# Performance work log

Measured on AMD Instinct MI355X. Metric: run time of the kernel, lower is better.

Reference implementation:

```python
import jax, jax.numpy as jnp
import numpy as np


def setup_inputs() -> dict:
    key = jax.random.key(0)
    k1, k2, k3, k4, k5 = jax.random.split(key, 5)
    B, C, H, W = 2, 3, 64, 64
    f_tar = jax.random.normal(k1, (B, C, H, W), dtype=jnp.float32)
    f_src = jax.random.normal(k2, (B, C, H, W), dtype=jnp.float32)
    # Pinhole intrinsics (focal=50, principal point at image center) + small noise,
    # guaranteed invertible.
    K_base = jnp.array([[50.0, 0.0, 32.0], [0.0, 50.0, 32.0], [0.0, 0.0, 1.0]],
                       dtype=jnp.float32)
    K = K_base[None] + 0.05 * jax.random.normal(k3, (B, 3, 3), dtype=jnp.float32)
    # Near-identity rotation-like matrix.
    R = jnp.eye(3, dtype=jnp.float32)[None] + 0.1 * jax.random.normal(
        k4, (B, 3, 3), dtype=jnp.float32)
    t = jax.random.normal(k5, (B, 3, 1), dtype=jnp.float32)
    return {"f_tar": f_tar, "f_src": f_src, "K": K, "R": R, "t": t}


def reference(f_tar, f_src, K, R, t):
    B, C, H, W = f_src.shape  # C == 3 (required by the cross product)
    N = H * W
    dtype = f_src.dtype

    f_src_flat = f_src.reshape(B, C, N)  # (B, 3, N)
    f_tar_flat = f_tar.reshape(B, C, N)  # (B, 3, N)

    # A[b, i, j] = <f_src[:, i], f_tar[:, j]>  -> (B, N, N)
    A = jnp.einsum('bci,bcj->bij', f_src_flat, f_tar_flat)

    # Homogeneous pixel coordinates (3, N): rows of meshgrid(H, W, indexing='ij').
    ix, iy = jnp.meshgrid(jnp.arange(H), jnp.arange(W), indexing='ij')
    pix = jnp.stack([ix.reshape(-1), iy.reshape(-1), jnp.ones(N, dtype=jnp.int32)],
                    axis=0).astype(dtype)  # (3, N)

    K_inv = jnp.linalg.inv(K)  # (B, 3, 3)
    # tar_proj = K @ (R @ (K^-1 @ x) + t)   -> (B, 3, N)
    cam_rays = jnp.einsum('bij,jn->bin', K_inv, pix)
    tar_proj = jnp.einsum('bij,bjn->bin', K, jnp.einsum('bij,bjn->bin', R, cam_rays) + t)
    # Origin projects to K @ (R @ 0 + t) = K @ t, broadcast over N.
    o_proj = jnp.einsum('bij,bjn->bin', K, t)  # (B, 3, 1)

    diff = tar_proj - o_proj  # (B, 3, N)

    # Epipolar distance: || (f_src - o) x diff || / ||diff||, broadcast to (B, N, N).
    a = f_src_flat[:, :, :, None] - o_proj[:, :, :, None]  # (B, 3, N, 1)
    b = diff[:, :, None, :]                                 # (B, 3, 1, N)
    cross = jnp.cross(a, b, axis=1)                         # (B, 3, N, N)
    cross_norm = jnp.linalg.norm(cross, axis=1)             # (B, N, N)
    diff_norm = jnp.linalg.norm(diff, axis=1, keepdims=True)  # (B, 1, N)
    d_epipolar = cross_norm / diff_norm                     # (B, N, N)

    # 'sigmoid' in the original is nn.Softmax(dim=-1).
    EPI_THRESH = 0.5
    SHARPNESS = 50.0
    weight_map = 1.0 - jax.nn.softmax(SHARPNESS * (d_epipolar - EPI_THRESH), axis=-1)

    A_weighted = A * weight_map
    attention_map = jax.nn.softmax(A_weighted, axis=1)  # normalize over src positions

    # (B, N, N) @ (B, N, C) -> (B, N, C), then raw view back to (B, C, H, W)
    attended = jnp.einsum('bik,bck->bic', attention_map, f_src_flat)
    return attended.reshape(B, C, H, W)
```

## Files before the change

kernel.cpp:

```cpp
#include <hip/hip_runtime.h>
#include <hip/hip_bf16.h>

namespace {
constexpr int BB = 2;
constexpr int NN = 4096;

constexpr int OFF_SRC4 = 0;
constexpr int OFF_TAR4 = 4 * BB * NN;
constexpr int OFF_U4   = 8 * BB * NN;
constexpr int OFF_W4   = 12 * BB * NN;
constexpr int OFF_RINV = 16 * BB * NN;
constexpr int OFF_CS   = 17 * BB * NN;
constexpr int OFF_NMAX = 18 * BB * NN;
constexpr size_t OFF_E1B = (size_t)1 << 20;
constexpr size_t NHALF   = (size_t)BB * NN * NN;
constexpr size_t OFF_E2B = OFF_E1B + NHALF * 2;
constexpr float L2E = 1.4426950408889634f;
constexpr float S50 = 72.13475204444817f;
constexpr float BIAS = 10.0f;
}

__device__ __forceinline__ float fsqrt(float x) { return __builtin_amdgcn_sqrtf(x); }
__device__ __forceinline__ float ex2(float x) { return __builtin_amdgcn_exp2f(x); }
__device__ __forceinline__ float frcp(float x) { return __builtin_amdgcn_rcpf(x); }

__global__ __launch_bounds__(256) void k_setup(
    const float* __restrict__ fsrc, const float* __restrict__ ftar,
    const float* __restrict__ Kb, const float* __restrict__ Rb,
    const float* __restrict__ tb, float* __restrict__ ws) {
  int gid = blockIdx.x * blockDim.x + threadIdx.x;
  if (gid >= BB * NN) return;
  int b = gid >> 12;
  int n = gid & (NN - 1);

  float K[9], R[9], t3[3];
#pragma unroll
  for (int k = 0; k < 9; k++) { K[k] = Kb[b * 9 + k]; R[k] = Rb[b * 9 + k]; }
#pragma unroll
  for (int k = 0; k < 3; k++) t3[k] = tb[b * 3 + k];

  float c00 = K[4] * K[8] - K[5] * K[7];
  float c01 = K[5] * K[6] - K[3] * K[8];
  float c02 = K[3] * K[7] - K[4] * K[6];
  float det = K[0] * c00 + K[1] * c01 + K[2] * c02;
  float id = 1.0f / det;
  float Ki[9];
  Ki[0] = c00 * id; Ki[1] = (K[2] * K[7] - K[1] * K[8]) * id; Ki[2] = (K[1] * K[5] - K[2] * K[4]) * id;
  Ki[3] = c01 * id; Ki[4] = (K[0] * K[8] - K[2] * K[6]) * id; Ki[5] = (K[2] * K[3] - K[0] * K[5]) * id;
  Ki[6] = c02 * id; Ki[7] = (K[1] * K[6] - K[0] * K[7]) * id; Ki[8] = (K[0] * K[4] - K[1] * K[3]) * id;

  float RK[9];
#pragma unroll
  for (int i = 0; i < 3; i++)
#pragma unroll
    for (int j = 0; j < 3; j++)
      RK[i * 3 + j] = R[i * 3 + 0] * Ki[j] + R[i * 3 + 1] * Ki[3 + j] + R[i * 3 + 2] * Ki[6 + j];
  float M3[9];
#pragma unroll
  for (int i = 0; i < 3; i++)
#pragma unroll
    for (int j = 0; j < 3; j++)
      M3[i * 3 + j] = K[i * 3 + 0] * RK[j] + K[i * 3 + 1] * RK[3 + j] + K[i * 3 + 2] * RK[6 + j];
  float o0 = K[0] * t3[0] + K[1] * t3[1] + K[2] * t3[2];
  float o1 = K[3] * t3[0] + K[4] * t3[1] + K[5] * t3[2];
  float o2 = K[6] * t3[0] + K[7] * t3[1] + K[8] * t3[2];

  float sx = fsrc[b * 3 * NN + 0 * NN + n];
  float sy = fsrc[b * 3 * NN + 1 * NN + n];
  float sz = fsrc[b * 3 * NN + 2 * NN + n];
  float tx = ftar[b * 3 * NN + 0 * NN + n];
  float ty = ftar[b * 3 * NN + 1 * NN + n];
  float tz = ftar[b * 3 * NN + 2 * NN + n];

  float ux = sx - o0, uy = sy - o1, uz = sz - o2;
  float usq = ux * ux + uy * uy + uz * uz;

  float px = (float)(n >> 6), py = (float)(n & 63);
  float vx = M3[0] * px + M3[1] * py + M3[2];
  float vy = M3[3] * px + M3[4] * py + M3[5];
  float vz = M3[6] * px + M3[7] * py + M3[8];
  float invn = rsqrtf(vx * vx + vy * vy + vz * vz);

  float4* src4 = (float4*)(ws + OFF_SRC4);
  float4* tar4 = (float4*)(ws + OFF_TAR4);
  float4* u4 = (float4*)(ws + OFF_U4);
  float4* w4 = (float4*)(ws + OFF_W4);
  src4[gid] = make_float4(sx, sy, sz, 0.f);
  tar4[gid] = make_float4(tx, ty, tz, 0.f);
  u4[gid] = make_float4(ux, uy, uz, usq);
  w4[gid] = make_float4(vx * invn, vy * invn, vz * invn, 0.f);

  float ns = fsqrt(sx * sx + sy * sy + sz * sz);
#pragma unroll
  for (int off = 32; off; off >>= 1) ns = fmaxf(ns, __shfl_xor(ns, off));
  if ((threadIdx.x & 63) == 0)
    atomicMax((unsigned int*)(ws + OFF_NMAX + b), __float_as_uint(ns));
}

__global__ __launch_bounds__(256, 4) void k_pass1(float* __restrict__ ws) {
  __shared__ float sred[4][8];
  const float4* u4 = (const float4*)(ws + OFF_U4);
  const float4* w4 = (const float4*)(ws + OFF_W4);
  float* rinv = ws + OFF_RINV;
  _Float16* eh = (_Float16*)((char*)ws + OFF_E1B);
  int tid = threadIdx.x, wid = tid >> 6, lane = tid & 63;
  int g0 = blockIdx.x * 8;
  int b = g0 >> 12;

  float ux[8], uy[8], uz[8], us[8];
#pragma unroll
  for (int r = 0; r < 8; r++) {
    float4 u = u4[g0 + r];
    ux[r] = u.x; uy[r] = u.y; uz[r] = u.z; us[r] = u.w;
  }
  const float4* wb = w4 + b * NN;

  float mx[8] = {0.f, 0.f, 0.f, 0.f, 0.f, 0.f, 0.f, 0.f};
  for (int j = wid * 64 + lane; j < NN; j += 256) {
    float4 w = wb[j];
#pragma unroll
    for (int r = 0; r < 8; r++) {
      float dot = ux[r] * w.x + uy[r] * w.y + uz[r] * w.z;
      mx[r] = fmaxf(mx[r], us[r] - dot * dot);
    }
  }
#pragma unroll
  for (int off = 32; off; off >>= 1)
#pragma unroll
    for (int r = 0; r < 8; r++) mx[r] = fmaxf(mx[r], __shfl_xor(mx[r], off));
  if (lane == 0) {
#pragma unroll
    for (int r = 0; r < 8; r++) sred[wid][r] = mx[r];
  }
  __syncthreads();
  float m2[8];
#pragma unroll
  for (int r = 0; r < 8; r++)
    m2[r] = S50 * fsqrt(fmaxf(fmaxf(sred[0][r], sred[1][r]), fmaxf(sred[2][r], sred[3][r])));
  __syncthreads();

  float s[8] = {0.f, 0.f, 0.f, 0.f, 0.f, 0.f, 0.f, 0.f};
  for (int j = wid * 64 + lane; j < NN; j += 256) {
    float4 w = wb[j];
#pragma unroll
    for (int r = 0; r < 8; r++) {
      float dot = ux[r] * w.x + uy[r] * w.y + uz[r] * w.z;
      float d2 = fmaxf(us[r] - dot * dot, 0.f);
      float t = fsqrt(d2);
      float ev = ex2(fmaf(S50, t, -m2[r]));
      s[r] += ev;
      eh[(size_t)(g0 + r) * NN + j] = (_Float16)ev;
    }
  }
#pragma unroll
  for (int off = 32; off; off >>= 1)
#pragma unroll
    for (int r = 0; r < 8; r++) s[r] += __shfl_xor(s[r], off);
  if (lane == 0) {
#pragma unroll
    for (int r = 0; r < 8; r++) sred[wid][r] = s[r];
  }
  __syncthreads();
  if (tid < 8) {
    float tot = sred[0][tid] + sred[1][tid] + sred[2][tid] + sred[3][tid];
    rinv[g0 + tid] = 1.f / tot;
  }
}

__global__ __launch_bounds__(256, 8) void k_pass2(float* __restrict__ ws) {
  __shared__ float sS[4][64];
  const float4* src4 = (const float4*)(ws + OFF_SRC4);
  const float4* tar4 = (const float4*)(ws + OFF_TAR4);
  const float* rinv = ws + OFF_RINV;
  float* CS = ws + OFF_CS;
  const _Float16* eh = (const _Float16*)((char*)ws + OFF_E1B);
  _Float16* Eh = (_Float16*)((char*)ws + OFF_E2B);

  int tid = threadIdx.x, wid = tid >> 6, lane = tid & 63;
  int g = blockIdx.x >> 4;
  int c = blockIdx.x & 15;
  int gc = g * 64 + lane;
  int b = gc >> 12;
  int base = b * NN;
  int jloc = gc - base;
  float maxns = ws[OFF_NMAX + b];

  float4 tt = tar4[gc];
  float Cj = BIAS - maxns * L2E * fsqrt(tt.x * tt.x + tt.y * tt.y + tt.z * tt.z);
  float txl = tt.x * L2E, tyl = tt.y * L2E, tzl = tt.z * L2E;

  float S = 0.f;
  int i0 = c * 256 + wid * 64;
#pragma unroll 4
  for (int it = 0; it < 64; ++it) {
    int i = i0 + it;
    float4 sv = src4[base + i];
    float invd = rinv[base + i];
    float ev = (float)eh[(size_t)(base + i) * NN + jloc];
    float wgt = fmaf(-ev, invd, 1.f);
    float Ap = sv.x * txl + sv.y * tyl + sv.z * tzl;
    float Ev = ex2(fmaf(Ap, wgt, Cj));
    S += Ev;
    Eh[(size_t)(base + i) * NN + jloc] = (_Float16)Ev;
  }
  sS[wid][lane] = S;
  __syncthreads();
  if (wid == 0) {
    float tot = sS[0][lane] + sS[1][lane] + sS[2][lane] + sS[3][lane];
    atomicAdd(&CS[gc], tot);
  }
}

__global__ __launch_bounds__(256, 8) void k_pass3(const float* __restrict__ ws,
                                                  float* __restrict__ out) {
  __shared__ float sacc[4][12];
  const float4* src4 = (const float4*)(ws + OFF_SRC4);
  const float* CS = ws + OFF_CS;
  const _Float16* Eh = (const _Float16*)((const char*)ws + OFF_E2B);
  int tid = threadIdx.x, wid = tid >> 6, lane = tid & 63;
  int g0 = blockIdx.x * 4;
  int b = g0 >> 12;
  int base = b * NN;

  float acc[4][3];
#pragma unroll
  for (int r = 0; r < 4; r++) { acc[r][0] = 0.f; acc[r][1] = 0.f; acc[r][2] = 0.f; }

#pragma unroll 2
  for (int j = wid * 64 + lane; j < NN; j += 256) {
    float4 sj = src4[base + j];
    float invS = frcp(CS[base + j]);
#pragma unroll
    for (int r = 0; r < 4; r++) {
      float Ev = (float)Eh[(size_t)(g0 + r) * NN + j];
      float p = Ev * invS;
      acc[r][0] += p * sj.x;
      acc[r][1] += p * sj.y;
      acc[r][2] += p * sj.z;
    }
  }
#pragma unroll
  for (int off = 32; off; off >>= 1)
#pragma unroll
    for (int r = 0; r < 4; r++) {
      acc[r][0] += __shfl_xor(acc[r][0], off);
      acc[r][1] += __shfl_xor(acc[r][1], off);
      acc[r][2] += __shfl_xor(acc[r][2], off);
    }
  if (lane == 0) {
#pragma unroll
    for (int r = 0; r < 4; r++) {
      sacc[wid][r * 3 + 0] = acc[r][0];
      sacc[wid][r * 3 + 1] = acc[r][1];
      sacc[wid][r * 3 + 2] = acc[r][2];
    }
  }
  __syncthreads();
  if (tid < 12) {
    float v = sacc[0][tid] + sacc[1][tid] + sacc[2][tid] + sacc[3][tid];
    out[g0 * 3 + tid] = v;
  }
}

extern "C" void kernel_launch(void* const* d_in, const int* in_sizes, int n_in,
                              void* d_out, int out_size, void* d_ws, size_t ws_size,
                              hipStream_t stream) {
  (void)in_sizes; (void)n_in; (void)out_size; (void)ws_size;
  const float* ftar = (const float*)d_in[0];
  const float* fsrc = (const float*)d_in[1];
  const float* K = (const float*)d_in[2];
  const float* R = (const float*)d_in[3];
  const float* t = (const float*)d_in[4];
  float* ws = (float*)d_ws;
  float* out = (float*)d_out;

  hipMemsetAsync((char*)d_ws + (size_t)OFF_CS * sizeof(float), 0,
                 (size_t)(BB * NN + BB) * sizeof(float), stream);

  k_setup<<<dim3((BB * NN + 255) / 256), dim3(256), 0, stream>>>(fsrc, ftar, K, R, t, ws);
  k_pass1<<<dim3(1024), dim3(256), 0, stream>>>(ws);
  k_pass2<<<dim3(2048), dim3(256), 0, stream>>>(ws);
  k_pass3<<<dim3(2048), dim3(256), 0, stream>>>(ws, out);
}
```

Measured before the change: 142.9 us.

## Recompute epipolar softmax term in pass2 instead of storing fp16 matrix

Pass1 no longer writes the full B*N*N fp16 epipolar exponent matrix. It stores only the per-row max and inverse sum. Pass2 recomputes the distance and exponent from the u/w vectors, which removes a 64 MB write and a 64 MB read in exchange for an extra sqrt, exp2 and dot product per element. A small numerical difference is possible because the value is no longer rounded through fp16.

```diff
diff --git a/kernel.cpp b/kernel.cpp
--- a/kernel.cpp
+++ b/kernel.cpp
@@ -9,12 +9,10 @@
 constexpr int OFF_TAR4 = 4 * BB * NN;
 constexpr int OFF_U4   = 8 * BB * NN;
 constexpr int OFF_W4   = 12 * BB * NN;
-constexpr int OFF_RINV = 16 * BB * NN;
-constexpr int OFF_CS   = 17 * BB * NN;
-constexpr int OFF_NMAX = 18 * BB * NN;
-constexpr size_t OFF_E1B = (size_t)1 << 20;
-constexpr size_t NHALF   = (size_t)BB * NN * NN;
-constexpr size_t OFF_E2B = OFF_E1B + NHALF * 2;
+constexpr int OFF_ROW  = 16 * BB * NN;
+constexpr int OFF_CS   = 18 * BB * NN;
+constexpr int OFF_NMAX = 19 * BB * NN;
+constexpr size_t OFF_EB = (size_t)1 << 20;
 constexpr float L2E = 1.4426950408889634f;
 constexpr float S50 = 72.13475204444817f;
 constexpr float BIAS = 10.0f;
@@ -101,8 +99,7 @@
   __shared__ float sred[4][8];
   const float4* u4 = (const float4*)(ws + OFF_U4);
   const float4* w4 = (const float4*)(ws + OFF_W4);
-  float* rinv = ws + OFF_RINV;
-  _Float16* eh = (_Float16*)((char*)ws + OFF_E1B);
+  float2* rowst = (float2*)(ws + OFF_ROW);
   int tid = threadIdx.x, wid = tid >> 6, lane = tid & 63;
   int g0 = blockIdx.x * 8;
   int b = g0 >> 12;
@@ -147,9 +144,7 @@
       float dot = ux[r] * w.x + uy[r] * w.y + uz[r] * w.z;
       float d2 = fmaxf(us[r] - dot * dot, 0.f);
       float t = fsqrt(d2);
-      float ev = ex2(fmaf(S50, t, -m2[r]));
-      s[r] += ev;
-      eh[(size_t)(g0 + r) * NN + j] = (_Float16)ev;
+      s[r] += ex2(fmaf(S50, t, -m2[r]));
     }
   }
 #pragma unroll
@@ -163,18 +158,19 @@
   __syncthreads();
   if (tid < 8) {
     float tot = sred[0][tid] + sred[1][tid] + sred[2][tid] + sred[3][tid];
-    rinv[g0 + tid] = 1.f / tot;
+    rowst[g0 + tid] = make_float2(m2[tid], 1.f / tot);
   }
 }
 
 __global__ __launch_bounds__(256, 8) void k_pass2(float* __restrict__ ws) {
   __shared__ float sS[4][64];
+  const float4* u4 = (const float4*)(ws + OFF_U4);
+  const float4* w4 = (const float4*)(ws + OFF_W4);
   const float4* src4 = (const float4*)(ws + OFF_SRC4);
   const float4* tar4 = (const float4*)(ws + OFF_TAR4);
-  const float* rinv = ws + OFF_RINV;
+  const float2* rowst = (const float2*)(ws + OFF_ROW);
   float* CS = ws + OFF_CS;
-  const _Float16* eh = (const _Float16*)((char*)ws + OFF_E1B);
-  _Float16* Eh = (_Float16*)((char*)ws + OFF_E2B);
+  _Float16* Eh = (_Float16*)((char*)ws + OFF_EB);
 
   int tid = threadIdx.x, wid = tid >> 6, lane = tid & 63;
   int g = blockIdx.x >> 4;
@@ -185,6 +181,7 @@
   int jloc = gc - base;
   float maxns = ws[OFF_NMAX + b];
 
+  float4 wj = w4[gc];
   float4 tt = tar4[gc];
   float Cj = BIAS - maxns * L2E * fsqrt(tt.x * tt.x + tt.y * tt.y + tt.z * tt.z);
   float txl = tt.x * L2E, tyl = tt.y * L2E, tzl = tt.z * L2E;
@@ -194,10 +191,14 @@
 #pragma unroll 4
   for (int it = 0; it < 64; ++it) {
     int i = i0 + it;
+    float4 uv = u4[base + i];
     float4 sv = src4[base + i];
-    float invd = rinv[base + i];
-    float ev = (float)eh[(size_t)(base + i) * NN + jloc];
-    float wgt = fmaf(-ev, invd, 1.f);
+    float2 rs = rowst[base + i];
+    float dot = uv.x * wj.x + uv.y * wj.y + uv.z * wj.z;
+    float d2 = fmaxf(uv.w - dot * dot, 0.f);
+    float t = fsqrt(d2);
+    float ev = ex2(fmaf(S50, t, -rs.x));
+    float wgt = fmaf(-ev, rs.y, 1.f);
     float Ap = sv.x * txl + sv.y * tyl + sv.z * tzl;
     float Ev = ex2(fmaf(Ap, wgt, Cj));
     S += Ev;
@@ -216,7 +217,7 @@
   __shared__ float sacc[4][12];
   const float4* src4 = (const float4*)(ws + OFF_SRC4);
   const float* CS = ws + OFF_CS;
-  const _Float16* Eh = (const _Float16*)((const char*)ws + OFF_E2B);
+  const _Float16* Eh = (const _Float16*)((const char*)ws + OFF_EB);
   int tid = threadIdx.x, wid = tid >> 6, lane = tid & 63;
   int g0 = blockIdx.x * 4;
   int b = g0 >> 12;
```

Measured after the change: 164.3 us. 1.15x slower.
